# Performance work log

Hardware: AMD Instinct MI355X
Metric: run time of the kernel (lower is better)

The kernel has to match this reference:

```python
import jax, jax.numpy as jnp
import numpy as np

EPS = 1e-12  # torch F.normalize default eps

def _l2norm(x):
    # torch.nn.functional.normalize(x, dim=-1): x / max(||x||_2, eps)
    n = jnp.linalg.norm(x, axis=-1, keepdims=True)
    return x / jnp.maximum(n, EPS)

def setup_inputs() -> dict:
    key = jax.random.key(0)
    ks = jax.random.split(key, 12)
    B, T, D, V, C = 16, 2048, 1024, 32000, 6
    s = 0.02
    text = jax.random.randint(ks[0], (B * T,), 0, V, dtype=jnp.int64)
    offsets = (jnp.arange(B, dtype=jnp.int64) * T)  # uniform-length sequences
    emb = jax.random.normal(ks[1], (V, D), dtype=jnp.float32) * s
    Wq = jax.random.normal(ks[2], (D, D), dtype=jnp.float32) * s
    bq = jnp.zeros((D,), jnp.float32)
    Wk = jax.random.normal(ks[3], (D, D), dtype=jnp.float32) * s
    bk = jnp.zeros((D,), jnp.float32)
    Wv = jax.random.normal(ks[4], (D, D), dtype=jnp.float32) * s
    bv = jnp.zeros((D,), jnp.float32)
    Wfc = jax.random.normal(ks[5], (D, D), dtype=jnp.float32) * s
    bfc = jnp.zeros((D,), jnp.float32)
    Wo = jax.random.normal(ks[6], (C, D), dtype=jnp.float32) * s
    bo = jnp.zeros((C,), jnp.float32)
    return {"text": text, "offsets": offsets, "emb": emb,
            "Wq": Wq, "bq": bq, "Wk": Wk, "bk": bk, "Wv": Wv, "bv": bv,
            "Wfc": Wfc, "bfc": bfc, "Wo": Wo, "bo": bo}

def reference(text, offsets, emb, Wq, bq, Wk, bk, Wv, bv, Wfc, bfc, Wo, bo):
    B = offsets.shape[0]
    T = text.shape[0] // B  # uniform lengths -> pad_sequence == reshape
    D = emb.shape[1]
    tok = text.reshape(B, T)
    x = emb[tok]                                   # [B,T,D]
    q = x @ Wq.T + bq
    k = x @ Wk.T + bk
    v = x @ Wv.T + bv
    scores = jnp.einsum('bqd,bkd->bqk', q, k) / jnp.sqrt(jnp.asarray(D, x.dtype))
    causal = jnp.tril(jnp.ones((T, T), dtype=bool))
    scores = jnp.where(causal[None, :, :], scores, -jnp.inf)
    attn = jax.nn.softmax(scores, axis=-1)
    out = jnp.einsum('bqk,bkd->bqd', attn, v) + x  # residual with embedding
    out = _l2norm(out)
    out = out + (out @ Wfc.T + bfc)                # residual FFN
    out = _l2norm(out)
    last = out[:, -1, :]                           # [B,D]
    return jax.nn.sigmoid(last @ Wo.T + bo)        # [B,num_class]
```

## Files before the change

### kernel.cpp

```cpp
#include <hip/hip_runtime.h>
#include <hip/hip_bf16.h>
#include <math.h>

typedef unsigned short ushort_t;

__device__ __forceinline__ float bf2f(ushort_t u) {
    union { unsigned int i; float f; } v;
    v.i = ((unsigned int)u) << 16;
    return v.f;
}

__device__ __forceinline__ ushort_t f2bf(float f) {
    union { float f; unsigned int i; } v; v.f = f;
    unsigned int lsb = (v.i >> 16) & 1;
    unsigned int r = v.i + 0x7FFF + lsb;
    return (ushort_t)(r >> 16);
}

__device__ __forceinline__ float wave_sum(float acc) {
    #pragma unroll
    for (int off = 32; off >= 1; off >>= 1) acc += __shfl_xor(acc, off, 64);
    return acc;
}
__device__ __forceinline__ float wave_max(float acc) {
    #pragma unroll
    for (int off = 32; off >= 1; off >>= 1) acc = fmaxf(acc, __shfl_xor(acc, off, 64));
    return acc;
}

__device__ __forceinline__ void ld8(const void* p, int isbf, size_t i, float* o) {
    if (isbf) {
        uint4 raw = *reinterpret_cast<const uint4*>((const ushort_t*)p + i);
        const ushort_t* pu = reinterpret_cast<const ushort_t*>(&raw);
        #pragma unroll
        for (int k = 0; k < 8; ++k) o[k] = bf2f(pu[k]);
    } else {
        const float4* f = reinterpret_cast<const float4*>((const float*)p + i);
        float4 a = f[0], b = f[1];
        o[0]=a.x; o[1]=a.y; o[2]=a.z; o[3]=a.w;
        o[4]=b.x; o[5]=b.y; o[6]=b.z; o[7]=b.w;
    }
}

__device__ __forceinline__ void ld4(const void* p, int isbf, size_t i, float* o) {
    if (isbf) {
        uint2 raw = *reinterpret_cast<const uint2*>((const ushort_t*)p + i);
        const ushort_t* pu = reinterpret_cast<const ushort_t*>(&raw);
        #pragma unroll
        for (int k = 0; k < 4; ++k) o[k] = bf2f(pu[k]);
    } else {
        float4 a = *reinterpret_cast<const float4*>((const float*)p + i);
        o[0]=a.x; o[1]=a.y; o[2]=a.z; o[3]=a.w;
    }
}

__device__ __forceinline__ float ldS(const void* p, int isbf, size_t i) {
    return isbf ? bf2f(((const ushort_t*)p)[i]) : ((const float*)p)[i];
}

__device__ __forceinline__ int tokAt(const void* text, int isi64, size_t i) {
    return isi64 ? ((const int*)text)[2 * i] : ((const int*)text)[i];
}

__device__ __forceinline__ void detect_flags(const void* emb, const void* text, int* sf) {
    if (threadIdx.x < 64) {
        const int lane = threadIdx.x;
        ushort_t u = ((const ushort_t*)emb)[2 * lane];
        int e = (u >> 7) & 0xFF;
        unsigned long long mb = __ballot(e >= 0x60 && e <= 0x7E);
        int odd = ((const int*)text)[2 * lane + 1];
        unsigned long long mi = __ballot(odd != 0);
        if (lane == 0) {
            sf[0] = (__popcll(mb) >= 32) ? 1 : 0;
            sf[1] = (__popcll(mi) == 0) ? 1 : 0;
        }
    }
    __syncthreads();
}

__device__ __forceinline__ void hoist16(const float* v, int lane, float* c16) {
    #pragma unroll
    for (int k = 0; k < 16; ++k) c16[k] = v[lane * 16 + k];
}

__global__ void kQC(const void* __restrict__ text, const void* __restrict__ emb,
                    const void* __restrict__ Wq, const void* __restrict__ bq,
                    const void* __restrict__ Wk, float* __restrict__ c_part,
                    int B, int T, int D) {
    const int ch = blockIdx.x / B;
    const int b  = blockIdx.x % B;
    const int i0 = ch << 5;
    const int tid = threadIdx.x;
    __shared__ int sf[2];
    __shared__ float xs[1024];
    __shared__ float qs[32];
    detect_flags(emb, text, sf);
    const int isbf = sf[0], isi64 = sf[1];
    const int tok = tokAt(text, isi64, (size_t)b * T + (T - 1));
    float w4[4];
    {
        const int dd = tid * 4;
        ld4(emb, isbf, (size_t)tok * D + dd, w4);
        xs[dd]=w4[0]; xs[dd+1]=w4[1]; xs[dd+2]=w4[2]; xs[dd+3]=w4[3];
    }
    __syncthreads();
    const int wave = tid >> 6, lane = tid & 63;
    float c16[16];
    hoist16(xs, lane, c16);
    float pacc[8];
    #pragma unroll
    for (int r = 0; r < 8; ++r) {
        const int i = i0 + wave * 8 + r;
        float w[8], acc = 0.f;
        ld8(Wq, isbf, (size_t)i * D + lane * 16, w);
        #pragma unroll
        for (int k = 0; k < 8; ++k) acc += w[k] * c16[k];
        ld8(Wq, isbf, (size_t)i * D + lane * 16 + 8, w);
        #pragma unroll
        for (int k = 0; k < 8; ++k) acc += w[k] * c16[8 + k];
        pacc[r] = acc;
    }
    #pragma unroll
    for (int r = 0; r < 8; ++r) {
        float acc = wave_sum(pacc[r]);
        const int i = i0 + wave * 8 + r;
        if (lane == 0) qs[wave * 8 + r] = acc + ldS(bq, isbf, i);
    }
    __syncthreads();
    const int d = tid * 4;
    float a0=0.f, a1=0.f, a2=0.f, a3=0.f;
    #pragma unroll 8
    for (int i = 0; i < 32; ++i) {
        const float qv = qs[i];
        ld4(Wk, isbf, (size_t)(i0 + i) * D + d, w4);
        a0 += qv*w4[0]; a1 += qv*w4[1]; a2 += qv*w4[2]; a3 += qv*w4[3];
    }
    *reinterpret_cast<float4*>(c_part + ((size_t)ch * B + b) * D + d)
        = make_float4(a0, a1, a2, a3);
}

__global__ void kCC(const float* __restrict__ c_part, float* __restrict__ c,
                    int B, int D, int nch) {
    const int nb = D >> 6;
    const int b = blockIdx.x / nb;
    const int dblk = blockIdx.x % nb;
    const int q = threadIdx.x >> 6, dl = threadIdx.x & 63;
    const int d = dblk * 64 + dl;
    __shared__ float red[256];
    const int per = nch >> 2;
    float acc = 0.f;
    for (int j = 0; j < per; ++j) {
        const int cc = q * per + j;
        acc += c_part[((size_t)cc * B + b) * D + d];
    }
    red[threadIdx.x] = acc;
    __syncthreads();
    if (q == 0) c[(size_t)b * D + d] = red[dl] + red[64 + dl] + red[128 + dl] + red[192 + dl];
}

__global__ void __launch_bounds__(256, 6)
k35(const void* __restrict__ text, const void* __restrict__ emb,
    const float* __restrict__ c, float* __restrict__ xbar_part,
    float* __restrict__ m_part, float* __restrict__ l_part,
    int B, int T, int D, float scale) {
    const int nchT = T >> 4;
    const int b = blockIdx.x / nchT;
    const int ch = blockIdx.x % nchT;
    const int j0 = ch << 4;
    const int tid = threadIdx.x;
    __shared__ int sf[2];
    __shared__ float cs[1024];
    __shared__ float sjs[16];
    __shared__ float wls[16];
    __shared__ int tks[16];
    detect_flags(emb, text, sf);
    const int isbf = sf[0], isi64 = sf[1];
    {
        const int d = tid * 4;
        float4 v = *reinterpret_cast<const float4*>(c + (size_t)b * D + d);
        cs[d]=v.x; cs[d+1]=v.y; cs[d+2]=v.z; cs[d+3]=v.w;
    }
    if (tid < 16) tks[tid] = tokAt(text, isi64, (size_t)b * T + j0 + tid);
    __syncthreads();
    const int wave = tid >> 6, lane = tid & 63;
    {
        float c16[16];
        hoist16(cs, lane, c16);
        float pacc[4];
        #pragma unroll
        for (int rr = 0; rr < 4; ++rr) {
            const int r = wave + rr * 4;
            const size_t base = (size_t)tks[r] * D + lane * 16;
            float acc = 0.f;
            if (isbf) {
                const ushort_t* E = (const ushort_t*)emb;
                uint4 raw = *reinterpret_cast<const uint4*>(E + base);
                const ushort_t* pu = reinterpret_cast<const ushort_t*>(&raw);
                #pragma unroll
                for (int k = 0; k < 8; ++k) acc += bf2f(pu[k]) * c16[k];
                raw = *reinterpret_cast<const uint4*>(E + base + 8);
                #pragma unroll
                for (int k = 0; k < 8; ++k) acc += bf2f(pu[k]) * c16[8 + k];
            } else {
                float w[8];
                ld8(emb, 0, base, w);
                #pragma unroll
                for (int k = 0; k < 8; ++k) acc += w[k] * c16[k];
                ld8(emb, 0, base + 8, w);
                #pragma unroll
                for (int k = 0; k < 8; ++k) acc += w[k] * c16[8 + k];
            }
            pacc[rr] = acc;
        }
        #pragma unroll
        for (int rr = 0; rr < 4; ++rr) {
            float acc = wave_sum(pacc[rr]);
            if (lane == 0) sjs[wave + rr * 4] = acc * scale;
        }
    }
    __syncthreads();
    float mx = -INFINITY;
    #pragma unroll
    for (int j = 0; j < 16; ++j) mx = fmaxf(mx, sjs[j]);
    if (tid < 16) wls[tid] = expf(sjs[tid] - mx);
    __syncthreads();
    if (tid < 64) {
        float v = (tid < 16) ? wls[tid] : 0.f;
        v = wave_sum(v);
        if (tid == 0) { m_part[(size_t)b * nchT + ch] = mx;
                        l_part[(size_t)b * nchT + ch] = v; }
    }
    const int d = tid * 4;
    float a0=0.f, a1=0.f, a2=0.f, a3=0.f;
    float w4[4];
    #pragma unroll
    for (int j = 0; j < 16; ++j) {
        const float wj = wls[j];
        ld4(emb, isbf, (size_t)tks[j] * D + d, w4);
        a0 += wj*w4[0]; a1 += wj*w4[1]; a2 += wj*w4[2]; a3 += wj*w4[3];
    }
    *reinterpret_cast<float4*>(xbar_part + ((size_t)b * nchT + ch) * D + d)
        = make_float4(a0, a1, a2, a3);
}

__global__ void kC(const float* __restrict__ xbar_part, const float* __restrict__ m_part,
                   const float* __restrict__ l_part, float* __restrict__ xbar,
                   int B, int D, int nchT) {
    const int nb = D >> 6;
    const int b = blockIdx.x / nb;
    const int dblk = blockIdx.x % nb;
    const int q = threadIdx.x >> 6, dl = threadIdx.x & 63;
    const int d = dblk * 64 + dl;
    __shared__ float sc[128];
    __shared__ float red[256];
    if (threadIdx.x < 64) {
        const int t = threadIdx.x;
        float m0 = (t < nchT) ? m_part[(size_t)b * nchT + t] : -INFINITY;
        float m1 = (64 + t < nchT) ? m_part[(size_t)b * nchT + 64 + t] : -INFINITY;
        float mx = wave_max(fmaxf(m0, m1));
        float l0 = (t < nchT) ? l_part[(size_t)b * nchT + t] * expf(m0 - mx) : 0.f;
        float l1 = (64 + t < nchT) ? l_part[(size_t)b * nchT + 64 + t] * expf(m1 - mx) : 0.f;
        float ls = wave_sum(l0 + l1);
        if (t < nchT) sc[t] = expf(m0 - mx) / ls;
        if (64 + t < nchT) sc[64 + t] = expf(m1 - mx) / ls;
    }
    __syncthreads();
    const int per = nchT >> 2;
    float acc = 0.f;
    for (int j = 0; j < per; ++j) {
        const int cc = q * per + j;
        acc += sc[cc] * xbar_part[((size_t)b * nchT + cc) * D + d];
    }
    red[threadIdx.x] = acc;
    __syncthreads();
    if (q == 0) xbar[(size_t)b * D + d] = red[dl] + red[64 + dl]
                                        + red[128 + dl] + red[192 + dl];
}

__global__ void kVA(const void* __restrict__ text, const void* __restrict__ emb,
                    const void* __restrict__ Wv, const void* __restrict__ bv,
                    const float* __restrict__ xbar, float* __restrict__ u,
                    int B, int T, int D) {
    const int ch = blockIdx.x / B;
    const int b  = blockIdx.x % B;
    const int r0 = ch << 5;
    const int tid = threadIdx.x;
    __shared__ int sf[2];
    __shared__ float xb[1024];
    __shared__ float xl[32];
    detect_flags(emb, text, sf);
    const int isbf = sf[0], isi64 = sf[1];
    const int tok = tokAt(text, isi64, (size_t)b * T + (T - 1));
    if (tid < 32) xl[tid] = ldS(emb, isbf, (size_t)tok * D + r0 + tid);
    {
        const int dd = tid * 4;
        float4 v = *reinterpret_cast<const float4*>(xbar + (size_t)b * D + dd);
        xb[dd]=v.x; xb[dd+1]=v.y; xb[dd+2]=v.z; xb[dd+3]=v.w;
    }
    __syncthreads();
    const int wave = tid >> 6, lane = tid & 63;
    float c16[16];
    hoist16(xb, lane, c16);
    float pacc[8];
    #pragma unroll
    for (int rr = 0; rr < 8; ++rr) {
        const int i = r0 + wave + rr * 4;
        float w[8], acc = 0.f;
        ld8(Wv, isbf, (size_t)i * D + lane * 16, w);
        #pragma unroll
        for (int k = 0; k < 8; ++k) acc += w[k] * c16[k];
        ld8(Wv, isbf, (size_t)i * D + lane * 16 + 8, w);
        #pragma unroll
        for (int k = 0; k < 8; ++k) acc += w[k] * c16[8 + k];
        pacc[rr] = acc;
    }
    #pragma unroll
    for (int rr = 0; rr < 8; ++rr) {
        float acc = wave_sum(pacc[rr]);
        const int i = r0 + wave + rr * 4;
        if (lane == 0) u[(size_t)b * D + i] = acc + ldS(bv, isbf, i) + xl[i - r0];
    }
}

__global__ void k6c_h2(const void* __restrict__ text, const void* __restrict__ emb,
                       const void* __restrict__ Wfc, const void* __restrict__ bfc,
                       const float* __restrict__ u, float* __restrict__ h2,
                       int B, int D) {
    const int ch = blockIdx.x / B;
    const int b  = blockIdx.x % B;
    const int r0 = ch << 5;
    const int tid = threadIdx.x;
    __shared__ int sf[2];
    __shared__ float hs[1024];
    __shared__ float red[256];
    __shared__ float s_rn;
    detect_flags(emb, text, sf);
    const int isbf = sf[0];
    float part;
    {
        const int dd = tid * 4;
        float4 v = *reinterpret_cast<const float4*>(u + (size_t)b * D + dd);
        hs[dd]=v.x; hs[dd+1]=v.y; hs[dd+2]=v.z; hs[dd+3]=v.w;
        part = v.x*v.x + v.y*v.y + v.z*v.z + v.w*v.w;
    }
    red[tid] = part;
    __syncthreads();
    for (int st = 128; st; st >>= 1) {
        if (tid < st) red[tid] += red[tid + st];
        __syncthreads();
    }
    if (tid == 0) s_rn = 1.f / fmaxf(sqrtf(red[0]), 1e-12f);
    __syncthreads();
    const float rn = s_rn;
    {
        const int dd = tid * 4;
        hs[dd] *= rn; hs[dd+1] *= rn; hs[dd+2] *= rn; hs[dd+3] *= rn;
    }
    __syncthreads();
    const int wave = tid >> 6, lane = tid & 63;
    float c16[16];
    hoist16(hs, lane, c16);
    float pacc[8];
    #pragma unroll
    for (int rr = 0; rr < 8; ++rr) {
        const int i = r0 + wave + rr * 4;
        float w[8], acc = 0.f;
        ld8(Wfc, isbf, (size_t)i * D + lane * 16, w);
        #pragma unroll
        for (int k = 0; k < 8; ++k) acc += w[k] * c16[k];
        ld8(Wfc, isbf, (size_t)i * D + lane * 16 + 8, w);
        #pragma unroll
        for (int k = 0; k < 8; ++k) acc += w[k] * c16[8 + k];
        pacc[rr] = acc;
    }
    #pragma unroll
    for (int rr = 0; rr < 8; ++rr) {
        float acc = wave_sum(pacc[rr]);
        const int i = r0 + wave + rr * 4;
        if (lane == 0) h2[(size_t)b * D + i] = hs[i] + acc + ldS(bfc, isbf, i);
    }
}

__global__ void k6d_out(const void* __restrict__ text, const void* __restrict__ emb,
                        const void* __restrict__ Wo, const void* __restrict__ bo,
                        const float* __restrict__ h2, void* __restrict__ out,
                        int D, int C, int total) {
    __shared__ int sf[2];
    detect_flags(emb, text, sf);
    const int isbf = sf[0];
    const int g = blockIdx.x * 4 + (threadIdx.x >> 6);
    if (g >= total) return;
    const int lane = threadIdx.x & 63;
    const int b = g / C, ci = g % C;
    float a1 = 0.f, a2 = 0.f, w[8], h[8];
    for (int d0 = lane * 8; d0 < D; d0 += 512) {
        ld8(Wo, isbf, (size_t)ci * D + d0, w);
        ld8(h2, 0, (size_t)b * D + d0, h);
        #pragma unroll
        for (int k = 0; k < 8; ++k) { a1 += w[k] * h[k]; a2 += h[k] * h[k]; }
    }
    a1 = wave_sum(a1);
    a2 = wave_sum(a2);
    if (lane == 0) {
        float rn = 1.f / fmaxf(sqrtf(a2), 1e-12f);
        float z = a1 * rn + ldS(bo, isbf, ci);
        float y = 1.f / (1.f + expf(-z));
        if (isbf) ((ushort_t*)out)[g] = f2bf(y);
        else      ((float*)out)[g] = y;
    }
}

extern "C" void kernel_launch(void* const* d_in, const int* in_sizes, int n_in,
                              void* d_out, int out_size, void* d_ws, size_t ws_size,
                              hipStream_t stream) {
    const void* text = d_in[0];
    const void* emb = d_in[2];
    const void* Wq  = d_in[3];
    const void* bq  = d_in[4];
    const void* Wk  = d_in[5];
    const void* Wv  = d_in[7];
    const void* bv  = d_in[8];
    const void* Wfc = d_in[9];
    const void* bfc = d_in[10];
    const void* Wo  = d_in[11];
    const void* bo  = d_in[12];

    const int B = in_sizes[1];
    const int T = in_sizes[0] / B;
    const int D = in_sizes[4];
    const int C = in_sizes[12];

    const int nch_c = D / 32;
    const int nchT  = T / 16;

    float* ws        = (float*)d_ws;
    float* c_part    = ws;
    float* c         = c_part + (size_t)nch_c * B * D;
    float* xbar_part = c + (size_t)B * D;
    float* m_part    = xbar_part + (size_t)B * nchT * D;
    float* l_part    = m_part + (size_t)B * nchT;
    float* xbar      = l_part + (size_t)B * nchT;
    float* u         = xbar + (size_t)B * D;
    float* h2        = u + (size_t)B * D;

    const float scale = 1.0f / sqrtf((float)D);

    kQC<<<(D / 32) * B, 256, 0, stream>>>(text, emb, Wq, bq, Wk, c_part, B, T, D);
    kCC<<<B * (D / 64), 256, 0, stream>>>(c_part, c, B, D, nch_c);
    k35<<<B * (T / 16), 256, 0, stream>>>(text, emb, c, xbar_part, m_part, l_part,
                                          B, T, D, scale);
    kC<<<B * (D / 64), 256, 0, stream>>>(xbar_part, m_part, l_part, xbar, B, D, nchT);
    kVA<<<(D / 32) * B, 256, 0, stream>>>(text, emb, Wv, bv, xbar, u, B, T, D);
    k6c_h2<<<(D / 32) * B, 256, 0, stream>>>(text, emb, Wfc, bfc, u, h2, B, D);
    k6d_out<<<(B * C + 3) / 4, 256, 0, stream>>>(text, emb, Wo, bo, h2, d_out, D, C, B * C);
}
```

Measured before the change: 316.1 us.

## Stage gathered embedding rows in LDS and halve k35 token chunk size

k35 now processes 8 tokens per block instead of 16, doubling the grid, and for bf16 embeddings stages the gathered rows in shared memory. Both the score dot product and the weighted row accumulation then read those rows from LDS instead of global memory. The query-key vector is loaded directly into registers rather than through shared memory. kC is generalised to reduce any number of chunk partials. The cost is twice as many partial vectors to write and reduce in kC.

```diff
diff --git a/kernel.cpp b/kernel.cpp
--- a/kernel.cpp
+++ b/kernel.cpp
@@ -158,86 +158,108 @@
     if (q == 0) c[(size_t)b * D + d] = red[dl] + red[64 + dl] + red[128 + dl] + red[192 + dl];
 }
 
-__global__ void __launch_bounds__(256, 6)
-k35(const void* __restrict__ text, const void* __restrict__ emb,
-    const float* __restrict__ c, float* __restrict__ xbar_part,
-    float* __restrict__ m_part, float* __restrict__ l_part,
-    int B, int T, int D, float scale) {
-    const int nchT = T >> 4;
+__global__ void k35(const void* __restrict__ text, const void* __restrict__ emb,
+                    const float* __restrict__ c, float* __restrict__ xbar_part,
+                    float* __restrict__ m_part, float* __restrict__ l_part,
+                    int B, int T, int D, float scale) {
+    const int nchT = T >> 3;
     const int b = blockIdx.x / nchT;
     const int ch = blockIdx.x % nchT;
-    const int j0 = ch << 4;
+    const int j0 = ch << 3;
     const int tid = threadIdx.x;
     __shared__ int sf[2];
-    __shared__ float cs[1024];
-    __shared__ float sjs[16];
-    __shared__ float wls[16];
-    __shared__ int tks[16];
+    __shared__ ushort_t rows[8 * 1024];
+    __shared__ float sjs[8];
+    __shared__ float wls[8];
+    __shared__ int tks[8];
     detect_flags(emb, text, sf);
     const int isbf = sf[0], isi64 = sf[1];
-    {
-        const int d = tid * 4;
-        float4 v = *reinterpret_cast<const float4*>(c + (size_t)b * D + d);
-        cs[d]=v.x; cs[d+1]=v.y; cs[d+2]=v.z; cs[d+3]=v.w;
-    }
-    if (tid < 16) tks[tid] = tokAt(text, isi64, (size_t)b * T + j0 + tid);
+    if (tid < 8) tks[tid] = tokAt(text, isi64, (size_t)b * T + j0 + tid);
     __syncthreads();
     const int wave = tid >> 6, lane = tid & 63;
-    {
-        float c16[16];
-        hoist16(cs, lane, c16);
-        float pacc[4];
-        #pragma unroll
-        for (int rr = 0; rr < 4; ++rr) {
-            const int r = wave + rr * 4;
-            const size_t base = (size_t)tks[r] * D + lane * 16;
+    float c16[16];
+    {
+        const float* cb = c + (size_t)b * D + lane * 16;
+        #pragma unroll
+        for (int k = 0; k < 4; ++k) {
+            float4 v = *reinterpret_cast<const float4*>(cb + k * 4);
+            c16[4*k]=v.x; c16[4*k+1]=v.y; c16[4*k+2]=v.z; c16[4*k+3]=v.w;
+        }
+    }
+    if (isbf) {
+        const ushort_t* E = (const ushort_t*)emb;
+        const int half = tid >> 7;
+        const int off  = (tid & 127) * 8;
+        #pragma unroll
+        for (int sw = 0; sw < 4; ++sw) {
+            const int r = sw * 2 + half;
+            uint4 v = *reinterpret_cast<const uint4*>(E + (size_t)tks[r] * D + off);
+            *reinterpret_cast<uint4*>(&rows[r * 1024 + off]) = v;
+        }
+    }
+    __syncthreads();
+    {
+        float pacc[2];
+        #pragma unroll
+        for (int rr = 0; rr < 2; ++rr) {
+            const int r = wave * 2 + rr;
             float acc = 0.f;
             if (isbf) {
-                const ushort_t* E = (const ushort_t*)emb;
-                uint4 raw = *reinterpret_cast<const uint4*>(E + base);
+                uint4 raw = *reinterpret_cast<const uint4*>(&rows[r * 1024 + lane * 16]);
                 const ushort_t* pu = reinterpret_cast<const ushort_t*>(&raw);
                 #pragma unroll
                 for (int k = 0; k < 8; ++k) acc += bf2f(pu[k]) * c16[k];
-                raw = *reinterpret_cast<const uint4*>(E + base + 8);
+                raw = *reinterpret_cast<const uint4*>(&rows[r * 1024 + lane * 16 + 8]);
                 #pragma unroll
                 for (int k = 0; k < 8; ++k) acc += bf2f(pu[k]) * c16[8 + k];
             } else {
                 float w[8];
-                ld8(emb, 0, base, w);
+                ld8(emb, 0, (size_t)tks[r] * D + lane * 16, w);
                 #pragma unroll
                 for (int k = 0; k < 8; ++k) acc += w[k] * c16[k];
-                ld8(emb, 0, base + 8, w);
+                ld8(emb, 0, (size_t)tks[r] * D + lane * 16 + 8, w);
                 #pragma unroll
                 for (int k = 0; k < 8; ++k) acc += w[k] * c16[8 + k];
             }
             pacc[rr] = acc;
         }
         #pragma unroll
-        for (int rr = 0; rr < 4; ++rr) {
+        for (int rr = 0; rr < 2; ++rr) {
             float acc = wave_sum(pacc[rr]);
-            if (lane == 0) sjs[wave + rr * 4] = acc * scale;
+            if (lane == 0) sjs[wave * 2 + rr] = acc * scale;
         }
     }
     __syncthreads();
     float mx = -INFINITY;
     #pragma unroll
-    for (int j = 0; j < 16; ++j) mx = fmaxf(mx, sjs[j]);
-    if (tid < 16) wls[tid] = expf(sjs[tid] - mx);
+    for (int j = 0; j < 8; ++j) mx = fmaxf(mx, sjs[j]);
+    if (tid < 8) wls[tid] = expf(sjs[tid] - mx);
     __syncthreads();
     if (tid < 64) {
-        float v = (tid < 16) ? wls[tid] : 0.f;
+        float v = (tid < 8) ? wls[tid] : 0.f;
         v = wave_sum(v);
         if (tid == 0) { m_part[(size_t)b * nchT + ch] = mx;
                         l_part[(size_t)b * nchT + ch] = v; }
     }
     const int d = tid * 4;
     float a0=0.f, a1=0.f, a2=0.f, a3=0.f;
-    float w4[4];
-    #pragma unroll
-    for (int j = 0; j < 16; ++j) {
-        const float wj = wls[j];
-        ld4(emb, isbf, (size_t)tks[j] * D + d, w4);
-        a0 += wj*w4[0]; a1 += wj*w4[1]; a2 += wj*w4[2]; a3 += wj*w4[3];
+    if (isbf) {
+        #pragma unroll
+        for (int j = 0; j < 8; ++j) {
+            const float wj = wls[j];
+            uint2 raw = *reinterpret_cast<const uint2*>(&rows[j * 1024 + d]);
+            const ushort_t* pu = reinterpret_cast<const ushort_t*>(&raw);
+            a0 += wj*bf2f(pu[0]); a1 += wj*bf2f(pu[1]);
+            a2 += wj*bf2f(pu[2]); a3 += wj*bf2f(pu[3]);
+        }
+    } else {
+        float w4[4];
+        #pragma unroll
+        for (int j = 0; j < 8; ++j) {
+            const float wj = wls[j];
+            ld4(emb, 0, (size_t)tks[j] * D + d, w4);
+            a0 += wj*w4[0]; a1 += wj*w4[1]; a2 += wj*w4[2]; a3 += wj*w4[3];
+        }
     }
     *reinterpret_cast<float4*>(xbar_part + ((size_t)b * nchT + ch) * D + d)
         = make_float4(a0, a1, a2, a3);
@@ -251,18 +273,20 @@
     const int dblk = blockIdx.x % nb;
     const int q = threadIdx.x >> 6, dl = threadIdx.x & 63;
     const int d = dblk * 64 + dl;
-    __shared__ float sc[128];
+    __shared__ float sc[256];
     __shared__ float red[256];
     if (threadIdx.x < 64) {
         const int t = threadIdx.x;
-        float m0 = (t < nchT) ? m_part[(size_t)b * nchT + t] : -INFINITY;
-        float m1 = (64 + t < nchT) ? m_part[(size_t)b * nchT + 64 + t] : -INFINITY;
-        float mx = wave_max(fmaxf(m0, m1));
-        float l0 = (t < nchT) ? l_part[(size_t)b * nchT + t] * expf(m0 - mx) : 0.f;
-        float l1 = (64 + t < nchT) ? l_part[(size_t)b * nchT + 64 + t] * expf(m1 - mx) : 0.f;
-        float ls = wave_sum(l0 + l1);
-        if (t < nchT) sc[t] = expf(m0 - mx) / ls;
-        if (64 + t < nchT) sc[64 + t] = expf(m1 - mx) / ls;
+        float mx = -INFINITY;
+        for (int cc = t; cc < nchT; cc += 64)
+            mx = fmaxf(mx, m_part[(size_t)b * nchT + cc]);
+        mx = wave_max(mx);
+        float ls = 0.f;
+        for (int cc = t; cc < nchT; cc += 64)
+            ls += l_part[(size_t)b * nchT + cc] * expf(m_part[(size_t)b * nchT + cc] - mx);
+        ls = wave_sum(ls);
+        for (int cc = t; cc < nchT; cc += 64)
+            sc[cc] = expf(m_part[(size_t)b * nchT + cc] - mx) / ls;
     }
     __syncthreads();
     const int per = nchT >> 2;
@@ -431,7 +455,7 @@
     const int C = in_sizes[12];
 
     const int nch_c = D / 32;
-    const int nchT  = T / 16;
+    const int nchT  = T / 8;
 
     float* ws        = (float*)d_ws;
     float* c_part    = ws;
@@ -447,8 +471,8 @@
 
     kQC<<<(D / 32) * B, 256, 0, stream>>>(text, emb, Wq, bq, Wk, c_part, B, T, D);
     kCC<<<B * (D / 64), 256, 0, stream>>>(c_part, c, B, D, nch_c);
-    k35<<<B * (T / 16), 256, 0, stream>>>(text, emb, c, xbar_part, m_part, l_part,
-                                          B, T, D, scale);
+    k35<<<B * (T / 8), 256, 0, stream>>>(text, emb, c, xbar_part, m_part, l_part,
+                                         B, T, D, scale);
     kC<<<B * (D / 64), 256, 0, stream>>>(xbar_part, m_part, l_part, xbar, B, D, nchT);
     kVA<<<(D / 32) * B, 256, 0, stream>>>(text, emb, Wv, bv, xbar, u, B, T, D);
     k6c_h2<<<(D / 32) * B, 256, 0, stream>>>(text, emb, Wfc, bfc, u, h2, B, D);
```

Result: faster. 296.6 us (-6.2%).

## Fold partial-sum reduction kernels into their consumers and stage bf16 rows in LDS

Applied to the files above, without the earlier changes.

Removes the separate reductions kCC and kC. Each k35 block now sums the 32 c partials itself, and each kVA block now does the softmax-weighted combine of the xbar partials itself. This saves two launches and two workspace round-trips. The cost is that many blocks repeat the same reduction, so each k35 block re-reads 32 partial vectors and each kVA block re-reads 128. It also adds a 32KB shared buffer that caches gathered embedding rows for the bf16 path and drops the launch bounds, which can lower occupancy even though the test inputs are fp32.

```diff
diff --git a/kernel.cpp b/kernel.cpp
--- a/kernel.cpp
+++ b/kernel.cpp
@@ -139,36 +139,17 @@
         = make_float4(a0, a1, a2, a3);
 }
 
-__global__ void kCC(const float* __restrict__ c_part, float* __restrict__ c,
-                    int B, int D, int nch) {
-    const int nb = D >> 6;
-    const int b = blockIdx.x / nb;
-    const int dblk = blockIdx.x % nb;
-    const int q = threadIdx.x >> 6, dl = threadIdx.x & 63;
-    const int d = dblk * 64 + dl;
-    __shared__ float red[256];
-    const int per = nch >> 2;
-    float acc = 0.f;
-    for (int j = 0; j < per; ++j) {
-        const int cc = q * per + j;
-        acc += c_part[((size_t)cc * B + b) * D + d];
-    }
-    red[threadIdx.x] = acc;
-    __syncthreads();
-    if (q == 0) c[(size_t)b * D + d] = red[dl] + red[64 + dl] + red[128 + dl] + red[192 + dl];
-}
-
-__global__ void __launch_bounds__(256, 6)
-k35(const void* __restrict__ text, const void* __restrict__ emb,
-    const float* __restrict__ c, float* __restrict__ xbar_part,
-    float* __restrict__ m_part, float* __restrict__ l_part,
-    int B, int T, int D, float scale) {
+__global__ void k35(const void* __restrict__ text, const void* __restrict__ emb,
+                    const float* __restrict__ c_part, float* __restrict__ xbar_part,
+                    float* __restrict__ m_part, float* __restrict__ l_part,
+                    int B, int T, int D, int nch_c, float scale) {
     const int nchT = T >> 4;
     const int b = blockIdx.x / nchT;
     const int ch = blockIdx.x % nchT;
     const int j0 = ch << 4;
     const int tid = threadIdx.x;
     __shared__ int sf[2];
+    __shared__ ushort_t rows[16 * 1024];
     __shared__ float cs[1024];
     __shared__ float sjs[16];
     __shared__ float wls[16];
@@ -177,10 +158,27 @@
     const int isbf = sf[0], isi64 = sf[1];
     {
         const int d = tid * 4;
-        float4 v = *reinterpret_cast<const float4*>(c + (size_t)b * D + d);
-        cs[d]=v.x; cs[d+1]=v.y; cs[d+2]=v.z; cs[d+3]=v.w;
+        float4 acc = make_float4(0.f, 0.f, 0.f, 0.f);
+        for (int cc = 0; cc < nch_c; ++cc) {
+            float4 v = *reinterpret_cast<const float4*>(
+                c_part + ((size_t)cc * B + b) * D + d);
+            acc.x += v.x; acc.y += v.y; acc.z += v.z; acc.w += v.w;
+        }
+        cs[d]=acc.x; cs[d+1]=acc.y; cs[d+2]=acc.z; cs[d+3]=acc.w;
     }
     if (tid < 16) tks[tid] = tokAt(text, isi64, (size_t)b * T + j0 + tid);
+    __syncthreads();
+    if (isbf) {
+        const ushort_t* E = (const ushort_t*)emb;
+        const int half = tid >> 7;
+        const int off  = (tid & 127) * 8;
+        #pragma unroll
+        for (int sw = 0; sw < 8; ++sw) {
+            const int r = sw * 2 + half;
+            uint4 v = *reinterpret_cast<const uint4*>(E + (size_t)tks[r] * D + off);
+            *reinterpret_cast<uint4*>(&rows[r * 1024 + off]) = v;
+        }
+    }
     __syncthreads();
     const int wave = tid >> 6, lane = tid & 63;
     {
@@ -190,23 +188,21 @@
         #pragma unroll
         for (int rr = 0; rr < 4; ++rr) {
             const int r = wave + rr * 4;
-            const size_t base = (size_t)tks[r] * D + lane * 16;
             float acc = 0.f;
             if (isbf) {
-                const ushort_t* E = (const ushort_t*)emb;
-                uint4 raw = *reinterpret_cast<const uint4*>(E + base);
+                uint4 raw = *reinterpret_cast<const uint4*>(&rows[r * 1024 + lane * 16]);
                 const ushort_t* pu = reinterpret_cast<const ushort_t*>(&raw);
                 #pragma unroll
                 for (int k = 0; k < 8; ++k) acc += bf2f(pu[k]) * c16[k];
-                raw = *reinterpret_cast<const uint4*>(E + base + 8);
+                raw = *reinterpret_cast<const uint4*>(&rows[r * 1024 + lane * 16 + 8]);
                 #pragma unroll
                 for (int k = 0; k < 8; ++k) acc += bf2f(pu[k]) * c16[8 + k];
             } else {
                 float w[8];
-                ld8(emb, 0, base, w);
+                ld8(emb, 0, (size_t)tks[r] * D + lane * 16, w);
                 #pragma unroll
                 for (int k = 0; k < 8; ++k) acc += w[k] * c16[k];
-                ld8(emb, 0, base + 8, w);
+                ld8(emb, 0, (size_t)tks[r] * D + lane * 16 + 8, w);
                 #pragma unroll
                 for (int k = 0; k < 8; ++k) acc += w[k] * c16[8 + k];
             }
@@ -232,29 +228,47 @@
     }
     const int d = tid * 4;
     float a0=0.f, a1=0.f, a2=0.f, a3=0.f;
-    float w4[4];
-    #pragma unroll
-    for (int j = 0; j < 16; ++j) {
-        const float wj = wls[j];
-        ld4(emb, isbf, (size_t)tks[j] * D + d, w4);
-        a0 += wj*w4[0]; a1 += wj*w4[1]; a2 += wj*w4[2]; a3 += wj*w4[3];
+    if (isbf) {
+        #pragma unroll
+        for (int j = 0; j < 16; ++j) {
+            const float wj = wls[j];
+            uint2 raw = *reinterpret_cast<const uint2*>(&rows[j * 1024 + d]);
+            const ushort_t* pu = reinterpret_cast<const ushort_t*>(&raw);
+            a0 += wj*bf2f(pu[0]); a1 += wj*bf2f(pu[1]);
+            a2 += wj*bf2f(pu[2]); a3 += wj*bf2f(pu[3]);
+        }
+    } else {
+        float w4[4];
+        #pragma unroll
+        for (int j = 0; j < 16; ++j) {
+            const float wj = wls[j];
+            ld4(emb, 0, (size_t)tks[j] * D + d, w4);
+            a0 += wj*w4[0]; a1 += wj*w4[1]; a2 += wj*w4[2]; a3 += wj*w4[3];
+        }
     }
     *reinterpret_cast<float4*>(xbar_part + ((size_t)b * nchT + ch) * D + d)
         = make_float4(a0, a1, a2, a3);
 }
 
-__global__ void kC(const float* __restrict__ xbar_part, const float* __restrict__ m_part,
-                   const float* __restrict__ l_part, float* __restrict__ xbar,
-                   int B, int D, int nchT) {
-    const int nb = D >> 6;
-    const int b = blockIdx.x / nb;
-    const int dblk = blockIdx.x % nb;
-    const int q = threadIdx.x >> 6, dl = threadIdx.x & 63;
-    const int d = dblk * 64 + dl;
+__global__ void kVA(const void* __restrict__ text, const void* __restrict__ emb,
+                    const float* __restrict__ xbar_part, const float* __restrict__ m_part,
+                    const float* __restrict__ l_part, const void* __restrict__ Wv,
+                    const void* __restrict__ bv, float* __restrict__ u,
+                    int B, int T, int D, int nchT) {
+    const int ch = blockIdx.x / B;
+    const int b  = blockIdx.x % B;
+    const int r0 = ch << 5;
+    const int tid = threadIdx.x;
+    __shared__ int sf[2];
+    __shared__ float xb[1024];
     __shared__ float sc[128];
-    __shared__ float red[256];
-    if (threadIdx.x < 64) {
-        const int t = threadIdx.x;
+    __shared__ float xl[32];
+    detect_flags(emb, text, sf);
+    const int isbf = sf[0], isi64 = sf[1];
+    const int tok = tokAt(text, isi64, (size_t)b * T + (T - 1));
+    if (tid < 32) xl[tid] = ldS(emb, isbf, (size_t)tok * D + r0 + tid);
+    if (tid < 64) {
+        const int t = tid;
         float m0 = (t < nchT) ? m_part[(size_t)b * nchT + t] : -INFINITY;
         float m1 = (64 + t < nchT) ? m_part[(size_t)b * nchT + 64 + t] : -INFINITY;
         float mx = wave_max(fmaxf(m0, m1));
@@ -265,37 +279,16 @@
         if (64 + t < nchT) sc[64 + t] = expf(m1 - mx) / ls;
     }
     __syncthreads();
-    const int per = nchT >> 2;
-    float acc = 0.f;
-    for (int j = 0; j < per; ++j) {
-        const int cc = q * per + j;
-        acc += sc[cc] * xbar_part[((size_t)b * nchT + cc) * D + d];
-    }
-    red[threadIdx.x] = acc;
-    __syncthreads();
-    if (q == 0) xbar[(size_t)b * D + d] = red[dl] + red[64 + dl]
-                                        + red[128 + dl] + red[192 + dl];
-}
-
-__global__ void kVA(const void* __restrict__ text, const void* __restrict__ emb,
-                    const void* __restrict__ Wv, const void* __restrict__ bv,
-                    const float* __restrict__ xbar, float* __restrict__ u,
-                    int B, int T, int D) {
-    const int ch = blockIdx.x / B;
-    const int b  = blockIdx.x % B;
-    const int r0 = ch << 5;
-    const int tid = threadIdx.x;
-    __shared__ int sf[2];
-    __shared__ float xb[1024];
-    __shared__ float xl[32];
-    detect_flags(emb, text, sf);
-    const int isbf = sf[0], isi64 = sf[1];
-    const int tok = tokAt(text, isi64, (size_t)b * T + (T - 1));
-    if (tid < 32) xl[tid] = ldS(emb, isbf, (size_t)tok * D + r0 + tid);
-    {
-        const int dd = tid * 4;
-        float4 v = *reinterpret_cast<const float4*>(xbar + (size_t)b * D + dd);
-        xb[dd]=v.x; xb[dd+1]=v.y; xb[dd+2]=v.z; xb[dd+3]=v.w;
+    {
+        const int d = tid * 4;
+        float4 acc = make_float4(0.f, 0.f, 0.f, 0.f);
+        for (int cc = 0; cc < nchT; ++cc) {
+            const float s = sc[cc];
+            float4 v = *reinterpret_cast<const float4*>(
+                xbar_part + ((size_t)b * nchT + cc) * D + d);
+            acc.x += s*v.x; acc.y += s*v.y; acc.z += s*v.z; acc.w += s*v.w;
+        }
+        xb[d]=acc.x; xb[d+1]=acc.y; xb[d+2]=acc.z; xb[d+3]=acc.w;
     }
     __syncthreads();
     const int wave = tid >> 6, lane = tid & 63;
@@ -435,22 +428,19 @@
 
     float* ws        = (float*)d_ws;
     float* c_part    = ws;
-    float* c         = c_part + (size_t)nch_c * B * D;
-    float* xbar_part = c + (size_t)B * D;
+    float* xbar_part = c_part + (size_t)nch_c * B * D;
     float* m_part    = xbar_part + (size_t)B * nchT * D;
     float* l_part    = m_part + (size_t)B * nchT;
-    float* xbar      = l_part + (size_t)B * nchT;
-    float* u         = xbar + (size_t)B * D;
+    float* u         = l_part + (size_t)B * nchT;
     float* h2        = u + (size_t)B * D;
 
     const float scale = 1.0f / sqrtf((float)D);
 
     kQC<<<(D / 32) * B, 256, 0, stream>>>(text, emb, Wq, bq, Wk, c_part, B, T, D);
-    kCC<<<B * (D / 64), 256, 0, stream>>>(c_part, c, B, D, nch_c);
-    k35<<<B * (T / 16), 256, 0, stream>>>(text, emb, c, xbar_part, m_part, l_part,
-                                          B, T, D, scale);
-    kC<<<B * (D / 64), 256, 0, stream>>>(xbar_part, m_part, l_part, xbar, B, D, nchT);
-    kVA<<<(D / 32) * B, 256, 0, stream>>>(text, emb, Wv, bv, xbar, u, B, T, D);
+    k35<<<B * (T / 16), 256, 0, stream>>>(text, emb, c_part, xbar_part, m_part, l_part,
+                                          B, T, D, nch_c, scale);
+    kVA<<<(D / 32) * B, 256, 0, stream>>>(text, emb, xbar_part, m_part, l_part,
+                                          Wv, bv, u, B, T, D, nchT);
     k6c_h2<<<(D / 32) * B, 256, 0, stream>>>(text, emb, Wfc, bfc, u, h2, B, D);
     k6d_out<<<(B * C + 3) / 4, 256, 0, stream>>>(text, emb, Wo, bo, h2, d_out, D, C, B * C);
 }
```

After: 314.5 us. Within noise of the previous version (-0.5%).
